# Kernel tuning notes

Measured on AMD Instinct MI355X. Metric: run time of the kernel, lower is better.

## Reference

```python
import jax, jax.numpy as jnp
import numpy as np

V, D, B, T = 50257, 512, 64, 512
MEM, FWD = 64, 48
RETRO = MEM - FWD  # 16
EPS = 1e-5


def setup_inputs() -> dict:
    key = jax.random.key(0)
    ks = jax.random.split(key, 16)
    n = lambda i, shape: (jax.random.normal(ks[i], shape, jnp.float32) * 0.02)
    return dict(
        seq=jax.random.randint(ks[0], (B, T), 0, V),
        embed=n(1, (V, D)),
        ff_w1=n(2, (D, 2 * D)), ff_b1=jnp.zeros((2 * D,), jnp.float32),
        ff_w2=n(3, (2 * D, D)), ff_b2=jnp.zeros((D,), jnp.float32),
        ln_g=jnp.ones((D,), jnp.float32), ln_b=jnp.zeros((D,), jnp.float32),
        fg_w=n(4, (D,)), fg_b=jnp.zeros((), jnp.float32),
        nw_w1=n(5, (2 * D, D)), nw_b1=jnp.zeros((D,), jnp.float32),
        nw_w2=n(6, (D,)), nw_b2=jnp.zeros((), jnp.float32),
        wq=n(7, (D, D)), bq=jnp.zeros((D,), jnp.float32),
        wk=n(8, (D, D)), bk=jnp.zeros((D,), jnp.float32),
        wv=n(9, (D, D)), bv=jnp.zeros((D,), jnp.float32),
        wo=n(10, (D, D)), bo=jnp.zeros((D,), jnp.float32),
        rq_w=n(11, (D, D)), rq_b=jnp.zeros((D,), jnp.float32),
        out_w=n(12, (D, V)), out_b=jnp.zeros((V,), jnp.float32),
    )


def reference(seq, embed, ff_w1, ff_b1, ff_w2, ff_b2, ln_g, ln_b,
              fg_w, fg_b, nw_w1, nw_b1, nw_w2, nw_b2,
              wq, bq, wk, bk, wv, bv, wo, bo, rq_w, rq_b, out_w, out_b):
    Bz = seq.shape[0]
    # Encoder: embed -> FFN residual -> LayerNorm
    h0 = embed[seq]                                            # [B,T,D]
    ff = jax.nn.relu(h0 @ ff_w1 + ff_b1) @ ff_w2 + ff_b2
    x = h0 + ff
    mu = x.mean(-1, keepdims=True)
    var = ((x - mu) ** 2).mean(-1, keepdims=True)
    hidden = (x - mu) / jnp.sqrt(var + EPS) * ln_g + ln_b       # [B,T,D]

    cand = hidden[:, :-3, :]                                   # [B,n_cand,D]
    n_cand = cand.shape[1]
    # Forward-gate topk (sorted ascending, as in torch code)
    fwd_scores = cand @ fg_w + fg_b                            # [B,n_cand]
    _, fwd_idx = jax.lax.top_k(fwd_scores, FWD)
    fwd_idx = jnp.sort(fwd_idx, axis=1)                        # [B,FWD]
    fwd_h = jnp.take_along_axis(hidden, fwd_idx[:, :, None], axis=1)  # [B,FWD,D]

    # Condition 'D': MHA re-encode (1 head) of forward slots over full sequence
    q = fwd_h @ wq + bq                                        # [B,FWD,D]
    kk = hidden @ wk + bk                                      # [B,T,D]
    v = hidden @ wv + bv                                       # [B,T,D]
    attn = jax.nn.softmax(jnp.einsum('bkd,btd->bkt', q, kk) / jnp.sqrt(jnp.float32(D)), axis=-1)
    re_slots = jnp.einsum('bkt,btd->bkd', attn, v) @ wo + bo   # [B,FWD,D]

    # New-write gate over skipped candidates -> retro slots
    context = hidden.mean(1)                                   # [B,D]
    gi = jnp.concatenate([cand, jnp.broadcast_to(context[:, None, :], cand.shape)], axis=-1)
    gs = jax.nn.sigmoid(jax.nn.relu(gi @ nw_w1 + nw_b1) @ nw_w2 + nw_b2)  # [B,n_cand]
    fwd_mask = jnp.zeros((Bz, n_cand), jnp.float32).at[
        jnp.arange(Bz)[:, None], fwd_idx].set(1.0)
    masked = jnp.where(fwd_mask > 0, -1e9, gs)
    _, sel = jax.lax.top_k(masked, RETRO)                      # [B,RETRO], descending-score order
    retro_h = jnp.take_along_axis(hidden, sel[:, :, None], axis=1)  # [B,RETRO,D]

    memory = jnp.concatenate([re_slots, retro_h], axis=1)      # [B,MEM,D] (exactly full)
    mem_mask = jnp.ones((Bz, MEM), jnp.float32)

    # Read head
    qh = hidden[:, -2, :] @ rq_w + rq_b                        # [B,D]
    scores = jnp.einsum('bmd,bd->bm', memory, qh)
    scores = jnp.where(mem_mask == 0, -1e9, scores)
    a = jax.nn.softmax(scores, axis=-1)
    ctx = jnp.einsum('bm,bmd->bd', a, memory)
    return ctx @ out_w + out_b                                 # [B,V]
```

## Files before the change

### kernel.cpp

```cpp
#include <hip/hip_runtime.h>

typedef unsigned short u16;
typedef unsigned int u32;

#define VV 50257
#define NCAND 509
#define NFWD 48
#define NRETRO 16

typedef __attribute__((ext_vector_type(8))) short bf16x8;
typedef __attribute__((ext_vector_type(4))) float f32x4;

__device__ __forceinline__ float bf2f(u16 u) {
  union { u32 i; float f; } v; v.i = ((u32)u) << 16; return v.f;
}
__device__ __forceinline__ u16 f2bf(float f) {
  union { float f; u32 u; } v; v.f = f;
  u32 u = v.u; u += 0x7fffu + ((u >> 16) & 1u); return (u16)(u >> 16);
}
__device__ __forceinline__ u16 bft(float f) {
  union { float f; u32 u; } v; v.f = f; return (u16)(v.u >> 16);
}
__device__ __forceinline__ float ldsel(const void* p, size_t i, int isbf) {
  return isbf ? bf2f(((const u16*)p)[i]) : ((const float*)p)[i];
}

__device__ __forceinline__ void g2l16(const u16* g, u16* l) {
  __builtin_amdgcn_global_load_lds((const __attribute__((address_space(1))) u32*)g,
                                   (__attribute__((address_space(3))) u32*)l, 16, 0, 0);
}

__global__ void detect_k(const u32* __restrict__ w, int* __restrict__ flag) {
  int bf = 1;
  for (int i = 0; i < 16; ++i) {
    u32 b1 = (w[i] >> 8) & 0x7fu;
    if (!(b1 >= 0x30u && b1 < 0x40u)) bf = 0;
  }
  *flag = bf;
}

__global__ void sentinel_k(float* __restrict__ out, int n, float val) {
  int i = blockIdx.x * 256 + threadIdx.x;
  if (i < n) out[i] = val;
}

__global__ __launch_bounds__(256) void tsplit_k(const float* __restrict__ W,
                                                u16* __restrict__ Th, u16* __restrict__ Tl,
                                                int K, int N) {
  __shared__ float tt[32][33];
  int nt = N >> 5;
  int n0 = (blockIdx.x % nt) << 5;
  int k0 = (blockIdx.x / nt) << 5;
  int c = threadIdx.x & 31, r = threadIdx.x >> 5;
#pragma unroll
  for (int i = 0; i < 32; i += 8) tt[r + i][c] = W[(size_t)(k0 + r + i) * N + n0 + c];
  __syncthreads();
#pragma unroll
  for (int i = 0; i < 32; i += 8) {
    int n = n0 + r + i, k = k0 + c;
    float v = tt[c][r + i];
    u16 h = bft(v);
    int idx = n * K + (k & ~63) + ((k & 63) ^ ((n & 7) << 3));
    Th[idx] = h; Tl[idx] = f2bf(v - bf2f(h));
  }
}

__global__ __launch_bounds__(256) void gsplit_k(const float* __restrict__ embed,
                                                const int* __restrict__ seqp,
                                                u16* __restrict__ Ph, u16* __restrict__ Pl) {
  int g = blockIdx.x * 256 + threadIdx.x;
  int m = g >> 6, j8 = (g & 63) << 3;
  const float* s = embed + (size_t)seqp[m] * 512 + j8;
  float4 a = *(const float4*)s;
  float4 b = *(const float4*)(s + 4);
  u16 h0 = bft(a.x), h1 = bft(a.y), h2 = bft(a.z), h3 = bft(a.w);
  u16 h4 = bft(b.x), h5 = bft(b.y), h6 = bft(b.z), h7 = bft(b.w);
  uint4 hv, lv;
  hv.x = (u32)h0 | ((u32)h1 << 16); hv.y = (u32)h2 | ((u32)h3 << 16);
  hv.z = (u32)h4 | ((u32)h5 << 16); hv.w = (u32)h6 | ((u32)h7 << 16);
  lv.x = (u32)f2bf(a.x - bf2f(h0)) | ((u32)f2bf(a.y - bf2f(h1)) << 16);
  lv.y = (u32)f2bf(a.z - bf2f(h2)) | ((u32)f2bf(a.w - bf2f(h3)) << 16);
  lv.z = (u32)f2bf(b.x - bf2f(h4)) | ((u32)f2bf(b.y - bf2f(h5)) << 16);
  lv.w = (u32)f2bf(b.z - bf2f(h6)) | ((u32)f2bf(b.w - bf2f(h7)) << 16);
  int di = m * 512 + (j8 ^ ((m & 7) << 3));
  *(uint4*)&Ph[di] = hv;
  *(uint4*)&Pl[di] = lv;
}

template<int ADDM, int RELU, int ACC, int OUT>
__global__ __launch_bounds__(256) void mgemm_k(
    const u16* __restrict__ Ah, const u16* __restrict__ Al,
    const u16* __restrict__ Bh, const u16* __restrict__ Bl,
    int ldk, int koff,
    const float* __restrict__ biasf, int boff,
    const u16* __restrict__ Rh, const u16* __restrict__ Rl,
    const float* __restrict__ addf,
    float* __restrict__ Cf, u16* __restrict__ Cb,
    u16* __restrict__ Ohi, u16* __restrict__ Olo)
{
  __shared__ __align__(16) u16 lds[32768];
  int tid = threadIdx.x;
  int cpx = gridDim.x >> 3;
  int bid = blockIdx.x;
  int wg = (bid & 7) * cpx + (bid >> 3);
  int my = wg >> 2, nx = wg & 3;
  int m0 = my << 7, n0 = nx << 7;
  int lane = tid & 63, wid = tid >> 6;

  const u16* gw; int stw;
  if (wid == 0)      { gw = Ah + (size_t)m0 * 512;        stw = 512; }
  else if (wid == 1) { gw = Al + (size_t)m0 * 512;        stw = 512; }
  else if (wid == 2) { gw = Bh + (size_t)n0 * ldk + koff; stw = ldk; }
  else               { gw = Bl + (size_t)n0 * ldk + koff; stw = ldk; }
  const u16* gl = gw + (size_t)(lane >> 3) * stw + ((lane & 7) << 3);
  int lb = wid << 13;

  f32x4 acc[4][4] = {};
  int wr = wid >> 1, wc = wid & 1;
  int cl = lane & 15;
  int kq8 = (lane >> 4) << 3;
  int swz = (cl & 7) << 3;

  for (int k0 = 0; k0 < 512; k0 += 64) {
#pragma unroll
    for (int i = 0; i < 16; ++i)
      g2l16(gl + (size_t)(i << 3) * stw + k0, &lds[lb + (i << 9)]);
    __syncthreads();
#pragma unroll
    for (int kt = 0; kt < 2; ++kt) {
      int kA = ((kt << 5) + kq8) ^ swz;
      bf16x8 bh[4], blo[4];
#pragma unroll
      for (int i = 0; i < 4; ++i) {
        int ib = (((wc << 6) + (i << 4) + cl) << 6) + kA;
        bh[i]  = *(const bf16x8*)&lds[16384 + ib];
        blo[i] = *(const bf16x8*)&lds[24576 + ib];
      }
#pragma unroll
      for (int i2 = 0; i2 < 4; ++i2) {
        int ia = (((wr << 6) + (i2 << 4) + cl) << 6) + kA;
        bf16x8 ah  = *(const bf16x8*)&lds[ia];
        bf16x8 alo = *(const bf16x8*)&lds[8192 + ia];
#pragma unroll
        for (int j = 0; j < 4; ++j) {
          acc[i2][j] = __builtin_amdgcn_mfma_f32_16x16x32_bf16(ah,  bh[j],  acc[i2][j], 0, 0, 0);
          acc[i2][j] = __builtin_amdgcn_mfma_f32_16x16x32_bf16(alo, bh[j],  acc[i2][j], 0, 0, 0);
          acc[i2][j] = __builtin_amdgcn_mfma_f32_16x16x32_bf16(ah,  blo[j], acc[i2][j], 0, 0, 0);
        }
      }
    }
    __syncthreads();
  }

  int rq = (lane >> 4) << 2;
  int mb = m0 + (wr << 6);
  int nb = n0 + (wc << 6);
#pragma unroll
  for (int j = 0; j < 4; ++j) {
    int n = nb + (j << 4) + cl;
    float bi = biasf ? biasf[boff + n] : 0.f;
#pragma unroll
    for (int i2 = 0; i2 < 4; ++i2) {
#pragma unroll
      for (int r = 0; r < 4; ++r) {
        int m = mb + (i2 << 4) + rq + r;
        float v = acc[i2][j][r] + bi;
        if (ADDM == 1) {
          int ridx = m * 512 + (n ^ ((m & 7) << 3));
          v += bf2f(Rh[ridx]) + bf2f(Rl[ridx]);
        }
        if (ADDM == 2) v += addf[((m >> 9) << 9) + n];
        if (ACC) v += Cf[(size_t)m * 512 + n];
        if (RELU) v = fmaxf(v, 0.f);
        if (OUT == 0) Cf[(size_t)m * 512 + n] = v;
        else if (OUT == 1) Cb[(size_t)m * 512 + n] = f2bf(v);
        else if (OUT == 2) {
          u16 h = bft(v);
          int oidx = m * 512 + (n ^ ((m & 7) << 3));
          Ohi[oidx] = h; Olo[oidx] = f2bf(v - bf2f(h));
        } else {
          int r64 = (m * 43691) >> 21;
          int mm = (r64 << 6) + (m - r64 * 48);
          Cf[(size_t)mm * 512 + n] = v;
        }
      }
    }
  }
}

template<int AG, int ADDM, int RELU, int ACC, int OUTBF>
__global__ __launch_bounds__(256) void gemm_k(
    const float* __restrict__ A, int lda,
    const void* __restrict__ gbase, const int* __restrict__ gidx,
    const void* __restrict__ Bw, int ldb, size_t boff,
    const void* __restrict__ bias, size_t bias_eoff,
    const void* __restrict__ adg_base, const int* __restrict__ adg_idx, int adg_ld,
    const float* __restrict__ addf, int add_shift, int addf_ld,
    void* __restrict__ Cv, int ldc, int K,
    const int* __restrict__ flagp)
{
  __shared__ float As[16][68];
  __shared__ float Bs[16][68];
  int isbf = *flagp;
  int tid = threadIdx.x;
  int m0 = blockIdx.y * 64;
  int n0 = blockIdx.x * 64;
  int tx = tid & 15, ty = tid >> 4;
  int arow = tid >> 2;
  int akq  = (tid & 3) << 2;
  int bcol = tid & 63;
  int bk0  = tid >> 6;

  size_t a_off;
  if (AG) a_off = (size_t)gidx[m0 + arow] * (size_t)lda;
  else    a_off = (size_t)(m0 + arow) * (size_t)lda;

  float acc[4][4] = {};

  for (int k0 = 0; k0 < K; k0 += 16) {
    {
      float4 v = *(const float4*)(A + a_off + k0 + akq);
      As[akq + 0][arow] = v.x;
      As[akq + 1][arow] = v.y;
      As[akq + 2][arow] = v.z;
      As[akq + 3][arow] = v.w;
    }
    if (isbf) {
      const u16* bp = (const u16*)Bw + boff;
#pragma unroll
      for (int l = 0; l < 4; ++l) {
        int kb = bk0 + (l << 2);
        Bs[kb][bcol] = bf2f(bp[(size_t)(k0 + kb) * ldb + n0 + bcol]);
      }
    } else {
      const float* bp = (const float*)Bw + boff;
#pragma unroll
      for (int l = 0; l < 4; ++l) {
        int kb = bk0 + (l << 2);
        Bs[kb][bcol] = bp[(size_t)(k0 + kb) * ldb + n0 + bcol];
      }
    }
    __syncthreads();
#pragma unroll
    for (int k = 0; k < 16; ++k) {
      float4 a4 = *(const float4*)&As[k][ty << 2];
      float4 b4 = *(const float4*)&Bs[k][tx << 2];
      float a[4] = {a4.x, a4.y, a4.z, a4.w};
      float bv[4] = {b4.x, b4.y, b4.z, b4.w};
#pragma unroll
      for (int i = 0; i < 4; ++i)
#pragma unroll
        for (int j = 0; j < 4; ++j) acc[i][j] += a[i] * bv[j];
    }
    __syncthreads();
  }

  int mrow = m0 + (ty << 2);
  int ncol = n0 + (tx << 2);
  float bi4[4] = {0.f, 0.f, 0.f, 0.f};
  if (bias) {
#pragma unroll
    for (int j = 0; j < 4; ++j) bi4[j] = ldsel(bias, bias_eoff + ncol + j, isbf);
  }
#pragma unroll
  for (int i = 0; i < 4; ++i) {
    int m = mrow + i;
    float v[4];
#pragma unroll
    for (int j = 0; j < 4; ++j) v[j] = acc[i][j] + bi4[j];
// ... 59 lines not shown
    const u16* ph = Hh + (size_t)grow * 512;
    const u16* pl = Hl + (size_t)grow * 512;
    float s = 0.f;
#pragma unroll
    for (int d = 0; d < 8; ++d) {
      float hv = bf2f(ph[lx + d * 64]) + bf2f(pl[lx + d * 64]);
      ca[d] += hv;
      s += hv * wl[lane + d * 64];
    }
#pragma unroll
    for (int off = 32; off > 0; off >>= 1) s += __shfl_xor(s, off);
    if (lane == 0) out[bb * 512 + t0 + r] = s + bias;
  }
#pragma unroll
  for (int d = 0; d < 8; ++d) cred[wave][lane + d * 64] = ca[d];
  __syncthreads();
  for (int d = threadIdx.x; d < 512; d += 256)
    part[(size_t)((bb << 3) + blockIdx.x) * 512 + d] =
        cred[0][d] + cred[1][d] + cred[2][d] + cred[3][d];
}

template<int SIG>
__global__ __launch_bounds__(256) void score_k(const float* __restrict__ h,
                                               const void* __restrict__ w,
                                               const void* __restrict__ b,
                                               float* __restrict__ out,
                                               const int* __restrict__ flagp) {
  int isbf = *flagp;
  int bb = blockIdx.y; int t0 = blockIdx.x * 64;
  __shared__ float wl[512];
  for (int d = threadIdx.x; d < 512; d += 256) wl[d] = ldsel(w, d, isbf);
  __syncthreads();
  int wave = threadIdx.x >> 6, lane = threadIdx.x & 63;
  float bias = ldsel(b, 0, isbf);
  for (int r = wave; r < 64; r += 4) {
    const float* hp = h + ((size_t)bb * 512 + t0 + r) * 512;
    float s = 0.f;
#pragma unroll
    for (int d = 0; d < 8; ++d) s += hp[lane + d * 64] * wl[lane + d * 64];
#pragma unroll
    for (int off = 32; off > 0; off >>= 1) s += __shfl_xor(s, off);
    if (lane == 0) {
      float v = s + bias;
      if (SIG) v = 1.0f / (1.0f + expf(-v));
      out[bb * 512 + t0 + r] = v;
    }
  }
}

__global__ __launch_bounds__(256) void topk_fwd_k(const float* __restrict__ scores,
                                                  int* __restrict__ fwd_idx,
                                                  int* __restrict__ fwd_mask) {
  int b = blockIdx.x, tid = threadIdx.x;
  __shared__ float vals[512];
  __shared__ float rv[256];
  __shared__ int   ri[256];
  __shared__ int   selb[NFWD];
  for (int t = tid; t < 512; t += 256) {
    vals[t] = (t < NCAND) ? scores[b * 512 + t] : -3.0e38f;
    fwd_mask[b * 512 + t] = 0;
  }
  __syncthreads();
  for (int it = 0; it < NFWD; ++it) {
    float bv = -3.0e38f; int bi = 0x7fffffff;
    for (int t = tid; t < 512; t += 256) {
      float v = vals[t];
      if (v > bv || (v == bv && t < bi)) { bv = v; bi = t; }
    }
    rv[tid] = bv; ri[tid] = bi;
    __syncthreads();
    for (int s = 128; s > 0; s >>= 1) {
      if (tid < s) {
        float ov = rv[tid + s]; int oi = ri[tid + s];
        if (ov > rv[tid] || (ov == rv[tid] && oi < ri[tid])) { rv[tid] = ov; ri[tid] = oi; }
      }
      __syncthreads();
    }
    if (tid == 0) { selb[it] = ri[0]; vals[ri[0]] = -3.0e38f; }
    __syncthreads();
  }
  if (tid == 0) {
    for (int i = 1; i < NFWD; ++i) {
      int v = selb[i], j = i - 1;
      while (j >= 0 && selb[j] > v) { selb[j + 1] = selb[j]; --j; }
      selb[j + 1] = v;
    }
    for (int i = 0; i < NFWD; ++i) {
      fwd_idx[b * NFWD + i] = selb[i];
      fwd_mask[b * 512 + selb[i]] = 1;
    }
  }
}

__global__ __launch_bounds__(256) void topk_retro_k(const float* __restrict__ gs,
                                                    const int* __restrict__ fwd_mask,
                                                    int* __restrict__ sel) {
  int b = blockIdx.x, tid = threadIdx.x;
  __shared__ float vals[512];
  __shared__ float rv[256];
  __shared__ int   ri[256];
  for (int t = tid; t < 512; t += 256) {
    float v;
    if (t < NCAND) v = fwd_mask[b * 512 + t] ? -1.0e9f : gs[b * 512 + t];
    else v = -3.0e38f;
    vals[t] = v;
  }
  __syncthreads();
  for (int it = 0; it < NRETRO; ++it) {
    float bv = -3.0e38f; int bi = 0x7fffffff;
    for (int t = tid; t < 512; t += 256) {
      float v = vals[t];
      if (v > bv || (v == bv && t < bi)) { bv = v; bi = t; }
    }
    rv[tid] = bv; ri[tid] = bi;
    __syncthreads();
    for (int s = 128; s > 0; s >>= 1) {
      if (tid < s) {
        float ov = rv[tid + s]; int oi = ri[tid + s];
        if (ov > rv[tid] || (ov == rv[tid] && oi < ri[tid])) { rv[tid] = ov; ri[tid] = oi; }
      }
      __syncthreads();
    }
    if (tid == 0) { sel[b * NRETRO + it] = ri[0]; vals[ri[0]] = -3.0e38f; }
    __syncthreads();
  }
}

__global__ __launch_bounds__(512) void context_red_k(const float* __restrict__ part,
                                                     float* __restrict__ ctx) {
  int b = blockIdx.x, d = threadIdx.x;
  float s = 0.f;
#pragma unroll
  for (int c = 0; c < 8; ++c) s += part[(size_t)((b << 3) + c) * 512 + d];
  ctx[b * 512 + d] = s * (1.0f / 512.0f);
}

__global__ __launch_bounds__(256) void fwdh_gather_p(const u16* __restrict__ Hh,
                                                     const u16* __restrict__ Hl,
                                                     const int* __restrict__ fwd_idx,
                                                     u16* __restrict__ Fh, u16* __restrict__ Fl) {
  int idx = blockIdx.x * 256 + threadIdx.x;
  int d = idx & 511, r = idx >> 9;
  int b = r / NFWD, i = r % NFWD;
  int t = fwd_idx[b * NFWD + i];
  int srow = b * 512 + t;
  int si = srow * 512 + (d & ~63) + ((d & 63) ^ ((srow & 7) << 3));
  float v = bf2f(Hh[si]) + bf2f(Hl[si]);
  u16 h = bft(v);
  int di = r * 512 + (d & ~63) + ((d & 63) ^ ((r & 7) << 3));
  Fh[di] = h; Fl[di] = f2bf(v - bf2f(h));
}

__global__ __launch_bounds__(256) void retro_gather_p(const u16* __restrict__ Hh,
                                                      const u16* __restrict__ Hl,
                                                      const int* __restrict__ sel,
                                                      float* __restrict__ mem) {
  int idx = blockIdx.x * 256 + threadIdx.x;
  int d = idx & 511, r = idx >> 9, b = r >> 4, j = r & 15;
  int t = sel[b * NRETRO + j];
  int srow = b * 512 + t;
  int si = srow * 512 + (d & ~63) + ((d & 63) ^ ((srow & 7) << 3));
  mem[((size_t)b * 64 + NFWD + j) * 512 + d] = bf2f(Hh[si]) + bf2f(Hl[si]);
}

__global__ __launch_bounds__(256) void s_k(const float* __restrict__ q,
                                           const u16* __restrict__ kk,
                                           float* __restrict__ S) {
  int b = blockIdx.y, t0 = blockIdx.x * 64;
  int tid = threadIdx.x, tq = tid & 15, kq = tid >> 4;
  __shared__ float qs[16][49];
  __shared__ float ks[16][68];
  float acc[3][4] = {};
  for (int dc = 0; dc < 512; dc += 16) {
    for (int e = tid; e < 768; e += 256) {
      int d = e / 48, k2 = e % 48;
      qs[d][k2] = q[((size_t)b * 48 + k2) * 512 + dc + d];
    }
    for (int e = tid; e < 1024; e += 256) {
      int t = e >> 4, d = e & 15;
      ks[d][t] = bf2f(kk[((size_t)b * 512 + t0 + t) * 512 + dc + d]);
    }
    __syncthreads();
#pragma unroll
    for (int d = 0; d < 16; ++d) {
      float4 kv = *(const float4*)&ks[d][tq << 2];
#pragma unroll
      for (int j = 0; j < 3; ++j) {
        float qv = qs[d][kq * 3 + j];
        acc[j][0] += qv * kv.x; acc[j][1] += qv * kv.y;
        acc[j][2] += qv * kv.z; acc[j][3] += qv * kv.w;
      }
    }
    __syncthreads();
  }
  const float sc = 0.044194173824159216f;
#pragma unroll
  for (int j = 0; j < 3; ++j) {
    int k = kq * 3 + j;
    float4 o; o.x = acc[j][0] * sc; o.y = acc[j][1] * sc;
    o.z = acc[j][2] * sc; o.w = acc[j][3] * sc;
    *(float4*)&S[((size_t)b * 48 + k) * 512 + t0 + (tq << 2)] = o;
  }
}

__global__ __launch_bounds__(256) void softmax_k(float* __restrict__ S) {
  float* p = S + (size_t)blockIdx.x * 512;
  int tid = threadIdx.x;
  __shared__ float red[256];
  __shared__ float stat[2];
  float v0 = p[tid], v1 = p[tid + 256];
  red[tid] = fmaxf(v0, v1);
  __syncthreads();
  for (int s = 128; s > 0; s >>= 1) { if (tid < s) red[tid] = fmaxf(red[tid], red[tid + s]); __syncthreads(); }
  if (tid == 0) stat[0] = red[0];
  __syncthreads();
  float mx = stat[0];
  float e0 = expf(v0 - mx), e1 = expf(v1 - mx);
  red[tid] = e0 + e1;
  __syncthreads();
  for (int s = 128; s > 0; s >>= 1) { if (tid < s) red[tid] += red[tid + s]; __syncthreads(); }
  if (tid == 0) stat[1] = 1.0f / red[0];
  __syncthreads();
  float inv = stat[1];
  p[tid] = e0 * inv; p[tid + 256] = e1 * inv;
}

__global__ __launch_bounds__(256) void pv_k(const float* __restrict__ P,
                                            const u16* __restrict__ vvp,
                                            u16* __restrict__ Ph, u16* __restrict__ Pl) {
  int b = blockIdx.y, d0 = blockIdx.x * 64;
  int tid = threadIdx.x, dq = tid & 15, kq = tid >> 4;
  __shared__ float ps[16][49];
  __shared__ float vs[16][68];
  float acc[3][4] = {};
  for (int tc = 0; tc < 512; tc += 16) {
    for (int e = tid; e < 768; e += 256) {
      int t = e / 48, k2 = e % 48;
      ps[t][k2] = P[((size_t)b * 48 + k2) * 512 + tc + t];
    }
    for (int e = tid; e < 1024; e += 256) {
      int t = e >> 6, d = e & 63;
      vs[t][d] = bf2f(vvp[((size_t)b * 512 + tc + t) * 512 + d0 + d]);
    }
    __syncthreads();
#pragma unroll
    for (int t = 0; t < 16; ++t) {
      float4 vval = *(const float4*)&vs[t][dq << 2];
#pragma unroll
      for (int j = 0; j < 3; ++j) {
        float pp = ps[t][kq * 3 + j];
        acc[j][0] += pp * vval.x; acc[j][1] += pp * vval.y;
        acc[j][2] += pp * vval.z; acc[j][3] += pp * vval.w;
      }
    }
    __syncthreads();
  }
#pragma unroll
  for (int j = 0; j < 3; ++j) {
    int k = kq * 3 + j;
    int row = b * 48 + k;
    int c = (row & 7) << 3;
    int di = row * 512 + d0 + ((dq << 2) ^ c);
    float v0 = acc[j][0], v1 = acc[j][1], v2 = acc[j][2], v3 = acc[j][3];
    u16 h0 = bft(v0), h1 = bft(v1), h2 = bft(v2), h3 = bft(v3);
    uint2 hv, lv;
    hv.x = (u32)h0 | ((u32)h1 << 16); hv.y = (u32)h2 | ((u32)h3 << 16);
    lv.x = (u32)f2bf(v0 - bf2f(h0)) | ((u32)f2bf(v1 - bf2f(h1)) << 16);
    lv.y = (u32)f2bf(v2 - bf2f(h2)) | ((u32)f2bf(v3 - bf2f(h3)) << 16);
    *(uint2*)&Ph[di] = hv;
    *(uint2*)&Pl[di] = lv;
  }
}

__global__ __launch_bounds__(512) void qh_p_k(const u16* __restrict__ Hh,
                                              const u16* __restrict__ Hl,
                                              const float* __restrict__ rq_w,
                                              const float* __restrict__ rq_b,
                                              float* __restrict__ qh) {
  int b = blockIdx.x, d = threadIdx.x;
  __shared__ float hr[512];
  int row = b * 512 + 510;
  int idx = row * 512 + (d & ~63) + ((d & 63) ^ 48);
  hr[d] = bf2f(Hh[idx]) + bf2f(Hl[idx]);
  __syncthreads();
  float s = 0.f;
  for (int k = 0; k < 512; ++k) s += hr[k] * rq_w[(size_t)k * 512 + d];
  qh[b * 512 + d] = s + rq_b[d];
}

__global__ __launch_bounds__(512) void mem_attn_k(const float* __restrict__ mem,
                                                  const float* __restrict__ qh,
                                                  float* __restrict__ ctx,
                                                  float* __restrict__ ctxT) {
  int b = blockIdx.x, tid = threadIdx.x;
  __shared__ float qv[512];
  __shared__ float sc[64];
  qv[tid] = qh[b * 512 + tid];
  __syncthreads();
  if (tid < 64) {
    const float* mp = mem + ((size_t)b * 64 + tid) * 512;
    float s = 0.f;
    for (int d = 0; d < 512; ++d) s += mp[d] * qv[d];
    float mx = s;
#pragma unroll
    for (int off = 32; off > 0; off >>= 1) mx = fmaxf(mx, __shfl_xor(mx, off));
    float e = expf(s - mx);
    float sum = e;
#pragma unroll
    for (int off = 32; off > 0; off >>= 1) sum += __shfl_xor(sum, off);
    sc[tid] = e / sum;
  }
  __syncthreads();
  float a = 0.f;
  for (int m = 0; m < 64; ++m) a += sc[m] * mem[((size_t)b * 64 + m) * 512 + tid];
  ctx[b * 512 + tid] = a;
  ctxT[(size_t)tid * 64 + b] = a;
}

__global__ __launch_bounds__(256) void out_part_k(const float* __restrict__ ctxT,
                                                  const float* __restrict__ out_w,
                                                  float* __restrict__ P0,
                                                  float* __restrict__ P1) {
  int bid = blockIdx.x;
  int slab2 = (bid & 7) + ((bid >> 6) << 3);
  if (slab2 >= 394) return;
  int xslab = slab2 >> 1, kh = slab2 & 1;
  int bg = (bid >> 3) & 7;
  int n = xslab * 256 + threadIdx.x;
  int nc = n < VV ? n : VV - 1;
  int b0 = bg << 3;
  int k0 = kh << 8;
  float acc[8] = {};
  const float* wp = out_w + (size_t)k0 * VV;
#pragma unroll 8
  for (int k = 0; k < 256; ++k) {
    float w = wp[(size_t)k * VV + nc];
    const float* cp = ctxT + ((size_t)(k0 + k) << 6) + b0;
#pragma unroll
    for (int i = 0; i < 8; ++i) acc[i] += cp[i] * w;
  }
  float* dst = kh ? P1 : P0;
  if (n < VV) {
#pragma unroll
    for (int i = 0; i < 8; ++i) dst[(size_t)(b0 + i) * VV + n] = acc[i];
  }
}

__global__ __launch_bounds__(256) void out_comb_k(const float* __restrict__ P0,
                                                  const float* __restrict__ P1,
                                                  const float* __restrict__ ob,
                                                  float* __restrict__ out) {
  int b = blockIdx.y;
  int n = blockIdx.x * 256 + threadIdx.x;
  if (n < VV) {
    size_t i = (size_t)b * VV + n;
    out[i] = P0[i] + P1[i] + ob[n];
  }
}

extern "C" void kernel_launch(void* const* d_in, const int* in_sizes, int n_in,
                              void* d_out, int out_size, void* d_ws, size_t ws_size,
                              hipStream_t stream) {
  const int*  seq    = (const int*)d_in[0];
  const void* embed  = d_in[1];
  const void* ff_w1  = d_in[2];
  const void* ff_b1  = d_in[3];
  const void* ff_w2  = d_in[4];
  const void* ff_b2  = d_in[5];
  const void* ln_g   = d_in[6];
  const void* ln_b   = d_in[7];
  const void* fg_w   = d_in[8];
  const void* fg_b   = d_in[9];
  const void* nw_w1  = d_in[10];
  const void* nw_b1  = d_in[11];
  const void* nw_w2  = d_in[12];
  const void* nw_b2  = d_in[13];
  const void* wq     = d_in[14];
  const void* bq     = d_in[15];
  const void* wk     = d_in[16];
  const void* bk     = d_in[17];
  const void* wv     = d_in[18];
  const void* bv     = d_in[19];
  const void* wo     = d_in[20];
  const void* bo     = d_in[21];
  const void* rq_w   = d_in[22];
  const void* rq_b   = d_in[23];
  const void* out_w  = d_in[24];
  const void* out_b  = d_in[25];
  float* out = (float*)d_out;

  float* ws = (float*)d_ws;
  float* hidden = ws;
  float* g1f    = ws;
  u16*   kku    = (u16*)ws;
  u16*   vvu    = (u16*)(ws + 8388608);
  float* P0     = ws;
  float* P1     = ws + 3216448;
  u16* actHh = (u16*)(ws + 16777216);
  u16* actHl = actHh + 8388608;
  u16* h0h   = (u16*)(ws + 25165824);
  u16* h0l   = h0h + 8388608;
  u16* Hh    = (u16*)(ws + 16777216);
  u16* Hl    = Hh + 16777216;
  size_t S0 = 33554432;
  float* fwd_scores = ws + S0;
  float* gs         = ws + S0 + 32768;
  float* context    = ws + S0 + 65536;
  float* gate_bias  = ws + S0 + 98304;
  float* qh         = ws + S0 + 131072;
  float* ctx        = ws + S0 + 163840;
  int*   fwd_idx    = (int*)(ws + S0 + 196608);
  int*   sel        = (int*)(ws + S0 + 199680);
  int*   fwd_mask   = (int*)(ws + S0 + 200704);
  int*   flagp      = (int*)(ws + S0 + 233472);
  float* cpart      = ws + S0 + 262144;
  u16*   Fh         = (u16*)(ws + S0 + 262144);
  u16*   Fl         = Fh + 1572864;
  float* q          = ws + S0 + 1835008;
  float* Smat       = ws + S0 + 3407872;
  u16* W0   = (u16*)(ws + S0 + 3407872);
  u16* WTnh = W0;            u16* WTnl = W0 + 262144;
  u16* WTkh = W0 + 524288;   u16* WTkl = W0 + 786432;
  u16* WTvh = W0 + 1048576;  u16* WTvl = W0 + 1310720;
  u16* WT1h = W0 + 1572864;  u16* WT1l = W0 + 2097152;
  u16* WT2h = W0 + 2621440;  u16* WT2l = W0 + 3145728;
  u16* Ph   = (u16*)(ws + S0 + 4980736);
  u16* Pl   = Ph + 1572864;
  u16* Wq0  = (u16*)(ws + S0 + 6553600);
  u16* WTqh = Wq0;          u16* WTql = Wq0 + 262144;
  u16* WToh = Wq0 + 524288; u16* WTol = Wq0 + 786432;
  float* memory = ws + S0 + 8126464;
  float* ctxT   = fwd_scores;
  const size_t NEED = (size_t)(33554432 + 10223616) * 4;

  if (ws_size < NEED) {
    float val = 500.0f + (float)(ws_size >> 20);
    sentinel_k<<<(out_size + 255) / 256, 256, 0, stream>>>(out, out_size, val);
    return;
  }

  detect_k<<<1, 1, 0, stream>>>((const u32*)embed, flagp);

  tsplit_k<<<512, 256, 0, stream>>>((const float*)ff_w1, WT1h, WT1l, 512, 1024);
  tsplit_k<<<512, 256, 0, stream>>>((const float*)ff_w2, WT2h, WT2l, 1024, 512);
  tsplit_k<<<256, 256, 0, stream>>>((const float*)nw_w1, WTnh, WTnl, 512, 512);
  tsplit_k<<<256, 256, 0, stream>>>((const float*)wk,    WTkh, WTkl, 512, 512);
  tsplit_k<<<256, 256, 0, stream>>>((const float*)wv,    WTvh, WTvl, 512, 512);
  tsplit_k<<<256, 256, 0, stream>>>((const float*)wq,    WTqh, WTql, 512, 512);
  tsplit_k<<<256, 256, 0, stream>>>((const float*)wo,    WToh, WTol, 512, 512);

  for (int mc = 0; mc < 2; ++mc) {
    const int* seqp = seq + mc * 16384;
    float* hid = hidden + (size_t)mc * 16384 * 512;
    gsplit_k<<<4096, 256, 0, stream>>>((const float*)embed, seqp, h0h, h0l);
    mgemm_k<0,1,0,2><<<512, 256, 0, stream>>>(h0h, h0l, WT1h, WT1l, 512, 0,
        (const float*)ff_b1, 0, nullptr, nullptr, nullptr,
        nullptr, nullptr, actHh, actHl);
    mgemm_k<0,0,0,0><<<512, 256, 0, stream>>>(actHh, actHl, WT2h, WT2l, 1024, 0,
        nullptr, 0, nullptr, nullptr, nullptr,
        hid, nullptr, nullptr, nullptr);
    mgemm_k<0,1,0,2><<<512, 256, 0, stream>>>(h0h, h0l, WT1h + 512*512, WT1l + 512*512, 512, 0,
        (const float*)ff_b1, 512, nullptr, nullptr, nullptr,
        nullptr, nullptr, actHh, actHl);
    mgemm_k<1,0,1,0><<<512, 256, 0, stream>>>(actHh, actHl, WT2h, WT2l, 1024, 512,
        (const float*)ff_b2, 0, h0h, h0l, nullptr,
        hid, nullptr, nullptr, nullptr);
  }
  ln_split_k<<<32768, 256, 0, stream>>>(hidden, (const float*)ln_g, (const float*)ln_b, Hh, Hl);
  gatectx_k<<<dim3(8,64), 256, 0, stream>>>(Hh, Hl, (const float*)fg_w, (const float*)fg_b,
                                            fwd_scores, cpart);
  topk_fwd_k<<<64, 256, 0, stream>>>(fwd_scores, fwd_idx, fwd_mask);
  context_red_k<<<64, 512, 0, stream>>>(cpart, context);
  gemm_k<0,0,0,0,0><<<dim3(8,1), 256, 0, stream>>>(
      context, 512, nullptr, nullptr, nw_w1, 512, (size_t)512*512, nw_b1, 0,
      nullptr, nullptr, 0, nullptr, 0, 0, gate_bias, 512, 512, flagp);
  mgemm_k<2,1,0,0><<<1024, 256, 0, stream>>>(Hh, Hl, WTnh, WTnl, 512, 0,
      nullptr, 0, nullptr, nullptr, gate_bias,
      g1f, nullptr, nullptr, nullptr);
  score_k<1><<<dim3(8,64), 256, 0, stream>>>(g1f, nw_w2, nw_b2, gs, flagp);
  topk_retro_k<<<64, 256, 0, stream>>>(gs, fwd_mask, sel);
  retro_gather_p<<<2048, 256, 0, stream>>>(Hh, Hl, sel, memory);
  fwdh_gather_p<<<6144, 256, 0, stream>>>(Hh, Hl, fwd_idx, Fh, Fl);
  mgemm_k<0,0,0,0><<<96, 256, 0, stream>>>(Fh, Fl, WTqh, WTql, 512, 0,
      (const float*)bq, 0, nullptr, nullptr, nullptr,
      q, nullptr, nullptr, nullptr);
  mgemm_k<0,0,0,1><<<1024, 256, 0, stream>>>(Hh, Hl, WTkh, WTkl, 512, 0,
      (const float*)bk, 0, nullptr, nullptr, nullptr,
      nullptr, kku, nullptr, nullptr);
  mgemm_k<0,0,0,1><<<1024, 256, 0, stream>>>(Hh, Hl, WTvh, WTvl, 512, 0,
      (const float*)bv, 0, nullptr, nullptr, nullptr,
      nullptr, vvu, nullptr, nullptr);
  s_k<<<dim3(8,64), 256, 0, stream>>>(q, kku, Smat);
  softmax_k<<<3072, 256, 0, stream>>>(Smat);
  pv_k<<<dim3(8,64), 256, 0, stream>>>(Smat, vvu, Ph, Pl);
  mgemm_k<0,0,0,3><<<96, 256, 0, stream>>>(Ph, Pl, WToh, WTol, 512, 0,
      (const float*)bo, 0, nullptr, nullptr, nullptr,
      memory, nullptr, nullptr, nullptr);
  qh_p_k<<<64, 512, 0, stream>>>(Hh, Hl, (const float*)rq_w, (const float*)rq_b, qh);
  mem_attn_k<<<64, 512, 0, stream>>>(memory, qh, ctx, ctxT);
  out_part_k<<<3200, 256, 0, stream>>>(ctxT, (const float*)out_w, P0, P1);
  out_comb_k<<<dim3(197,64), 256, 0, stream>>>(P0, P1, (const float*)out_b, out);
}
```

Baseline: 1.254 ms.

## Fuse FFN and K/V GEMMs, rank-based top-k, MFMA output projection

Generalizes the split-bf16 MFMA GEMM with N-tile count, K-steps and output stride. This lets the FFN run as one wide W1 GEMM and one full-K W2 GEMM over four M chunks, and lets K and V be computed by one concatenated GEMM. The iterative argmax top-k loops become a single-pass rank-counting selection. The fp32 output projection (partial sums plus combine) is replaced by a bf16-transposed out_w and an MFMA GEMM that uses a hi/lo split of ctx. The out_w transpose now runs on every call and out_w carries only a single bf16 term, which reduces precision on that operand.

```diff
diff --git a/kernel.cpp b/kernel.cpp
--- a/kernel.cpp
+++ b/kernel.cpp
@@ -63,6 +63,32 @@
     int idx = n * K + (k & ~63) + ((k & 63) ^ ((n & 7) << 3));
     Th[idx] = h; Tl[idx] = f2bf(v - bf2f(h));
   }
+}
+
+__global__ __launch_bounds__(256) void tout_k(const float* __restrict__ W,
+                                              u16* __restrict__ WoT) {
+  __shared__ float tt[32][33];
+  const int nt = 1572;
+  int n0 = (blockIdx.x % nt) << 5;
+  int k0 = (blockIdx.x / nt) << 5;
+  int c = threadIdx.x & 31, r = threadIdx.x >> 5;
+#pragma unroll
+  for (int i = 0; i < 32; i += 8) {
+    int n = n0 + c;
+    tt[r + i][c] = (n < VV) ? W[(size_t)(k0 + r + i) * VV + n] : 0.f;
+  }
+  __syncthreads();
+#pragma unroll
+  for (int i = 0; i < 32; i += 8) {
+    int n = n0 + r + i, k = k0 + c;
+    WoT[(size_t)n * 512 + (k & ~63) + ((k & 63) ^ ((n & 7) << 3))] = f2bf(tt[c][r + i]);
+  }
+}
+
+__global__ void concat2_k(const float* __restrict__ a, const float* __restrict__ b,
+                          float* __restrict__ o) {
+  int i = blockIdx.x * 256 + threadIdx.x;
+  if (i < 1024) o[i] = (i < 512) ? a[i] : b[i - 512];
 }
 
 __global__ __launch_bounds__(256) void gsplit_k(const float* __restrict__ embed,
@@ -87,31 +113,31 @@
   *(uint4*)&Pl[di] = lv;
 }
 
-template<int ADDM, int RELU, int ACC, int OUT>
+template<int NT, int KST, int ADDM, int RELU, int OUT>
 __global__ __launch_bounds__(256) void mgemm_k(
     const u16* __restrict__ Ah, const u16* __restrict__ Al,
     const u16* __restrict__ Bh, const u16* __restrict__ Bl,
-    int ldk, int koff,
+    int lda, int ldb, int koff,
     const float* __restrict__ biasf, int boff,
     const u16* __restrict__ Rh, const u16* __restrict__ Rl,
     const float* __restrict__ addf,
     float* __restrict__ Cf, u16* __restrict__ Cb,
-    u16* __restrict__ Ohi, u16* __restrict__ Olo)
+    u16* __restrict__ Ohi, u16* __restrict__ Olo, int ldc)
 {
   __shared__ __align__(16) u16 lds[32768];
   int tid = threadIdx.x;
   int cpx = gridDim.x >> 3;
   int bid = blockIdx.x;
   int wg = (bid & 7) * cpx + (bid >> 3);
-  int my = wg >> 2, nx = wg & 3;
+  int my = wg / NT, nx = wg % NT;
   int m0 = my << 7, n0 = nx << 7;
   int lane = tid & 63, wid = tid >> 6;
 
   const u16* gw; int stw;
-  if (wid == 0)      { gw = Ah + (size_t)m0 * 512;        stw = 512; }
-  else if (wid == 1) { gw = Al + (size_t)m0 * 512;        stw = 512; }
-  else if (wid == 2) { gw = Bh + (size_t)n0 * ldk + koff; stw = ldk; }
-  else               { gw = Bl + (size_t)n0 * ldk + koff; stw = ldk; }
+  if (wid == 0)      { gw = Ah + (size_t)m0 * lda;        stw = lda; }
+  else if (wid == 1) { gw = Al + (size_t)m0 * lda;        stw = lda; }
+  else if (wid == 2) { gw = Bh + (size_t)n0 * ldb + koff; stw = ldb; }
+  else               { gw = Bl + (size_t)n0 * ldb + koff; stw = ldb; }
   const u16* gl = gw + (size_t)(lane >> 3) * stw + ((lane & 7) << 3);
   int lb = wid << 13;
 
@@ -121,7 +147,7 @@
   int kq8 = (lane >> 4) << 3;
   int swz = (cl & 7) << 3;
 
-  for (int k0 = 0; k0 < 512; k0 += 64) {
+  for (int k0 = 0; k0 < KST * 64; k0 += 64) {
 #pragma unroll
     for (int i = 0; i < 16; ++i)
       g2l16(gl + (size_t)(i << 3) * stw + k0, &lds[lb + (i << 9)]);
@@ -170,13 +196,12 @@
           v += bf2f(Rh[ridx]) + bf2f(Rl[ridx]);
         }
         if (ADDM == 2) v += addf[((m >> 9) << 9) + n];
-        if (ACC) v += Cf[(size_t)m * 512 + n];
         if (RELU) v = fmaxf(v, 0.f);
-        if (OUT == 0) Cf[(size_t)m * 512 + n] = v;
-        else if (OUT == 1) Cb[(size_t)m * 512 + n] = f2bf(v);
+        if (OUT == 0) Cf[(size_t)m * ldc + n] = v;
+        else if (OUT == 1) Cb[(size_t)m * ldc + n] = f2bf(v);
         else if (OUT == 2) {
           u16 h = bft(v);
-          int oidx = m * 512 + (n ^ ((m & 7) << 3));
+          size_t oidx = (size_t)m * ldc + (n & ~63) + ((n & 63) ^ ((m & 7) << 3));
           Ohi[oidx] = h; Olo[oidx] = f2bf(v - bf2f(h));
         } else {
           int r64 = (m * 43691) >> 21;
@@ -184,6 +209,70 @@
           Cf[(size_t)mm * 512 + n] = v;
         }
       }
+    }
+  }
+}
+
+__global__ __launch_bounds__(256) void out_mgemm_k(
+    const u16* __restrict__ ctxh, const u16* __restrict__ ctxl,
+    const u16* __restrict__ WoT, const float* __restrict__ ob,
+    float* __restrict__ out) {
+  __shared__ __align__(16) u16 lds[16384];
+  int tid = threadIdx.x;
+  int n0 = blockIdx.x << 7;
+  int lane = tid & 63, wid = tid >> 6;
+  const u16* gw; int lb0;
+  if (wid == 0)      { gw = ctxh;                         lb0 = 0; }
+  else if (wid == 1) { gw = ctxl;                         lb0 = 4096; }
+  else if (wid == 2) { gw = WoT + (size_t)n0 * 512;        lb0 = 8192; }
+  else               { gw = WoT + (size_t)(n0 + 64) * 512; lb0 = 12288; }
+  const u16* gl = gw + (size_t)(lane >> 3) * 512 + ((lane & 7) << 3);
+
+  f32x4 acc[4][2] = {};
+  int cl = lane & 15;
+  int kq8 = (lane >> 4) << 3;
+  int swz = (cl & 7) << 3;
+
+  for (int k0 = 0; k0 < 512; k0 += 64) {
+#pragma unroll
+    for (int i = 0; i < 8; ++i)
+      g2l16(gl + (size_t)(i << 3) * 512 + k0, &lds[lb0 + (i << 9)]);
+    __syncthreads();
+#pragma unroll
+    for (int kt = 0; kt < 2; ++kt) {
+      int kA = ((kt << 5) + kq8) ^ swz;
+      bf16x8 bw[2];
+#pragma unroll
+      for (int j = 0; j < 2; ++j) {
+        int rB = (wid << 5) + (j << 4) + cl;
+        bw[j] = *(const bf16x8*)&lds[8192 + (rB << 6) + kA];
+      }
+#pragma unroll
+      for (int i2 = 0; i2 < 4; ++i2) {
+        int ra = ((i2 << 4) + cl) << 6;
+        bf16x8 ah  = *(const bf16x8*)&lds[ra + kA];
+        bf16x8 alo = *(const bf16x8*)&lds[4096 + ra + kA];
+#pragma unroll
+        for (int j = 0; j < 2; ++j) {
+          acc[i2][j] = __builtin_amdgcn_mfma_f32_16x16x32_bf16(ah,  bw[j], acc[i2][j], 0, 0, 0);
+          acc[i2][j] = __builtin_amdgcn_mfma_f32_16x16x32_bf16(alo, bw[j], acc[i2][j], 0, 0, 0);
+        }
+      }
+    }
+    __syncthreads();
+  }
+
+  int rq = (lane >> 4) << 2;
+#pragma unroll
+  for (int j = 0; j < 2; ++j) {
+    int n = n0 + (wid << 5) + (j << 4) + cl;
+    if (n < VV) {
+      float bi = ob[n];
+#pragma unroll
+      for (int i2 = 0; i2 < 4; ++i2)
+#pragma unroll
+        for (int r = 0; r < 4; ++r)
+          out[(size_t)((i2 << 4) + rq + r) * VV + n] = acc[i2][j][r] + bi;
     }
   }
 }
@@ -211,10 +300,7 @@
   int bcol = tid & 63;
   int bk0  = tid >> 6;
 
-  size_t a_off;
-  if (AG) a_off = (size_t)gidx[m0 + arow] * (size_t)lda;
-  else    a_off = (size_t)(m0 + arow) * (size_t)lda;
-
+  size_t a_off = (size_t)(m0 + arow) * (size_t)lda;
   float acc[4][4] = {};
 
   for (int k0 = 0; k0 < K; k0 += 16) {
@@ -380,42 +466,37 @@
                                                   int* __restrict__ fwd_idx,
                                                   int* __restrict__ fwd_mask) {
   int b = blockIdx.x, tid = threadIdx.x;
-  __shared__ float vals[512];
-  __shared__ float rv[256];
-  __shared__ int   ri[256];
-  __shared__ int   selb[NFWD];
-  for (int t = tid; t < 512; t += 256) {
-    vals[t] = (t < NCAND) ? scores[b * 512 + t] : -3.0e38f;
-    fwd_mask[b * 512 + t] = 0;
-  }
-  __syncthreads();
-  for (int it = 0; it < NFWD; ++it) {
-    float bv = -3.0e38f; int bi = 0x7fffffff;
-    for (int t = tid; t < 512; t += 256) {
-      float v = vals[t];
-      if (v > bv || (v == bv && t < bi)) { bv = v; bi = t; }
-    }
-    rv[tid] = bv; ri[tid] = bi;
-    __syncthreads();
-    for (int s = 128; s > 0; s >>= 1) {
-      if (tid < s) {
-        float ov = rv[tid + s]; int oi = ri[tid + s];
-        if (ov > rv[tid] || (ov == rv[tid] && oi < ri[tid])) { rv[tid] = ov; ri[tid] = oi; }
-      }
-      __syncthreads();
-    }
-    if (tid == 0) { selb[it] = ri[0]; vals[ri[0]] = -3.0e38f; }
-    __syncthreads();
-  }
-  if (tid == 0) {
-    for (int i = 1; i < NFWD; ++i) {
-      int v = selb[i], j = i - 1;
-      while (j >= 0 && selb[j] > v) { selb[j + 1] = selb[j]; --j; }
-      selb[j + 1] = v;
-    }
-    for (int i = 0; i < NFWD; ++i) {
-      fwd_idx[b * NFWD + i] = selb[i];
-      fwd_mask[b * 512 + selb[i]] = 1;
+  __shared__ float sv[512];
+  __shared__ int flg[512];
+  for (int t = tid; t < 512; t += 256)
+    sv[t] = (t < NCAND) ? scores[b * 512 + t] : -3.0e38f;
+  __syncthreads();
+  const float4* sv4 = (const float4*)sv;
+#pragma unroll
+  for (int h = 0; h < 2; ++h) {
+    int t = tid + (h << 8);
+    float s = sv[t];
+    int cnt = 0;
+    for (int t2 = 0; t2 < 128; ++t2) {
+      float4 o = sv4[t2];
+      int base = t2 << 2;
+      cnt += (o.x > s) || (o.x == s && (base + 0) < t);
+      cnt += (o.y > s) || (o.y == s && (base + 1) < t);
+      cnt += (o.z > s) || (o.z == s && (base + 2) < t);
+      cnt += (o.w > s) || (o.w == s && (base + 3) < t);
+    }
+    int f = (cnt < NFWD) ? 1 : 0;
+    flg[t] = f;
+    fwd_mask[b * 512 + t] = f;
+  }
+  __syncthreads();
+#pragma unroll
+  for (int h = 0; h < 2; ++h) {
+    int t = tid + (h << 8);
+    if (flg[t]) {
+      int pos = 0;
+      for (int t2 = 0; t2 < t; ++t2) pos += flg[t2];
+      fwd_idx[b * NFWD + pos] = t;
     }
   }
 }
@@ -424,33 +505,29 @@
                                                     const int* __restrict__ fwd_mask,
                                                     int* __restrict__ sel) {
   int b = blockIdx.x, tid = threadIdx.x;
-  __shared__ float vals[512];
-  __shared__ float rv[256];
-  __shared__ int   ri[256];
+  __shared__ float sv[512];
   for (int t = tid; t < 512; t += 256) {
     float v;
     if (t < NCAND) v = fwd_mask[b * 512 + t] ? -1.0e9f : gs[b * 512 + t];
     else v = -3.0e38f;
-    vals[t] = v;
-  }
-  __syncthreads();
-  for (int it = 0; it < NRETRO; ++it) {
-    float bv = -3.0e38f; int bi = 0x7fffffff;
-    for (int t = tid; t < 512; t += 256) {
-      float v = vals[t];
-      if (v > bv || (v == bv && t < bi)) { bv = v; bi = t; }
-    }
-    rv[tid] = bv; ri[tid] = bi;
-    __syncthreads();
-    for (int s = 128; s > 0; s >>= 1) {
-      if (tid < s) {
-        float ov = rv[tid + s]; int oi = ri[tid + s];
-        if (ov > rv[tid] || (ov == rv[tid] && oi < ri[tid])) { rv[tid] = ov; ri[tid] = oi; }
-      }
-      __syncthreads();
-    }
-    if (tid == 0) { sel[b * NRETRO + it] = ri[0]; vals[ri[0]] = -3.0e38f; }
-    __syncthreads();
+    sv[t] = v;
+  }
+  __syncthreads();
+  const float4* sv4 = (const float4*)sv;
+#pragma unroll
+  for (int h = 0; h < 2; ++h) {
+    int t = tid + (h << 8);
+    float s = sv[t];
+    int cnt = 0;
+    for (int t2 = 0; t2 < 128; ++t2) {
+      float4 o = sv4[t2];
+      int base = t2 << 2;
+      cnt += (o.x > s) || (o.x == s && (base + 0) < t);
+      cnt += (o.y > s) || (o.y == s && (base + 1) < t);
+      cnt += (o.z > s) || (o.z == s && (base + 2) < t);
+      cnt += (o.w > s) || (o.w == s && (base + 3) < t);
+    }
+    if (cnt < NRETRO) sel[b * NRETRO + cnt] = t;
   }
 }
 
@@ -506,7 +583,7 @@
     }
     for (int e = tid; e < 1024; e += 256) {
       int t = e >> 4, d = e & 15;
-      ks[d][t] = bf2f(kk[((size_t)b * 512 + t0 + t) * 512 + dc + d]);
+      ks[d][t] = bf2f(kk[((size_t)b * 512 + t0 + t) * 1024 + dc + d]);
     }
     __syncthreads();
 #pragma unroll
@@ -568,7 +645,7 @@
     }
     for (int e = tid; e < 1024; e += 256) {
       int t = e >> 6, d = e & 63;
-      vs[t][d] = bf2f(vvp[((size_t)b * 512 + tc + t) * 512 + d0 + d]);
+      vs[t][d] = bf2f(vvp[((size_t)b * 512 + tc + t) * 1024 + d0 + d]);
     }
     __syncthreads();
 #pragma unroll
@@ -618,8 +695,8 @@
 
 __global__ __launch_bounds__(512) void mem_attn_k(const float* __restrict__ mem,
                                                   const float* __restrict__ qh,
-                                                  float* __restrict__ ctx,
-                                                  float* __restrict__ ctxT) {
+                                                  u16* __restrict__ ctxh,
+                                                  u16* __restrict__ ctxl) {
   int b = blockIdx.x, tid = threadIdx.x;
   __shared__ float qv[512];
   __shared__ float sc[64];
@@ -641,49 +718,9 @@
   __syncthreads();
   float a = 0.f;
   for (int m = 0; m < 64; ++m) a += sc[m] * mem[((size_t)b * 64 + m) * 512 + tid];
-  ctx[b * 512 + tid] = a;
-  ctxT[(size_t)tid * 64 + b] = a;
-}
-
-__global__ __launch_bounds__(256) void out_part_k(const float* __restrict__ ctxT,
-                                                  const float* __restrict__ out_w,
-                                                  float* __restrict__ P0,
-                                                  float* __restrict__ P1) {
-  int bid = blockIdx.x;
-  int slab2 = (bid & 7) + ((bid >> 6) << 3);
-  if (slab2 >= 394) return;
-  int xslab = slab2 >> 1, kh = slab2 & 1;
-  int bg = (bid >> 3) & 7;
-  int n = xslab * 256 + threadIdx.x;
-  int nc = n < VV ? n : VV - 1;
-  int b0 = bg << 3;
-  int k0 = kh << 8;
-  float acc[8] = {};
-  const float* wp = out_w + (size_t)k0 * VV;
-#pragma unroll 8
-  for (int k = 0; k < 256; ++k) {
-    float w = wp[(size_t)k * VV + nc];
-    const float* cp = ctxT + ((size_t)(k0 + k) << 6) + b0;
-#pragma unroll
-    for (int i = 0; i < 8; ++i) acc[i] += cp[i] * w;
-  }
-  float* dst = kh ? P1 : P0;
-  if (n < VV) {
-#pragma unroll
-    for (int i = 0; i < 8; ++i) dst[(size_t)(b0 + i) * VV + n] = acc[i];
-  }
-}
-
-__global__ __launch_bounds__(256) void out_comb_k(const float* __restrict__ P0,
-                                                  const float* __restrict__ P1,
-                                                  const float* __restrict__ ob,
-                                                  float* __restrict__ out) {
-  int b = blockIdx.y;
-  int n = blockIdx.x * 256 + threadIdx.x;
-  if (n < VV) {
-    size_t i = (size_t)b * VV + n;
-    out[i] = P0[i] + P1[i] + ob[n];
-  }
+  int di = b * 512 + (tid & ~63) + ((tid & 63) ^ ((b & 7) << 3));
+  u16 h = bft(a);
+  ctxh[di] = h; ctxl[di] = f2bf(a - bf2f(h));
 }
 
 extern "C" void kernel_launch(void* const* d_in, const int* in_sizes, int n_in,
@@ -720,45 +757,43 @@
   float* ws = (float*)d_ws;
   float* hidden = ws;
   float* g1f    = ws;
-  u16*   kku    = (u16*)ws;
-  u16*   vvu    = (u16*)(ws + 8388608);
-  float* P0     = ws;
-  float* P1     = ws + 3216448;
-  u16* actHh = (u16*)(ws + 16777216);
+  u16*   kvu    = (u16*)ws;
+  u16* h0h   = (u16*)(ws + 16777216);
+  u16* h0l   = h0h + 4194304;
+  u16* actHh = (u16*)(ws + 20971520);
   u16* actHl = actHh + 8388608;
-  u16* h0h   = (u16*)(ws + 25165824);
-  u16* h0l   = h0h + 8388608;
   u16* Hh    = (u16*)(ws + 16777216);
   u16* Hl    = Hh + 16777216;
+  u16* WoT   = (u16*)(ws + 16777216);
   size_t S0 = 33554432;
   float* fwd_scores = ws + S0;
   float* gs         = ws + S0 + 32768;
   float* context    = ws + S0 + 65536;
   float* gate_bias  = ws + S0 + 98304;
   float* qh         = ws + S0 + 131072;
-  float* ctx        = ws + S0 + 163840;
+  u16*   ctxh       = (u16*)(ws + S0 + 163840);
+  u16*   ctxl       = ctxh + 32768;
   int*   fwd_idx    = (int*)(ws + S0 + 196608);
   int*   sel        = (int*)(ws + S0 + 199680);
   int*   fwd_mask   = (int*)(ws + S0 + 200704);
   int*   flagp      = (int*)(ws + S0 + 233472);
+  float* bkv        = ws + S0 + 236544;
   float* cpart      = ws + S0 + 262144;
   u16*   Fh         = (u16*)(ws + S0 + 262144);
   u16*   Fl         = Fh + 1572864;
   float* q          = ws + S0 + 1835008;
   float* Smat       = ws + S0 + 3407872;
-  u16* W0   = (u16*)(ws + S0 + 3407872);
-  u16* WTnh = W0;            u16* WTnl = W0 + 262144;
-  u16* WTkh = W0 + 524288;   u16* WTkl = W0 + 786432;
-  u16* WTvh = W0 + 1048576;  u16* WTvl = W0 + 1310720;
-  u16* WT1h = W0 + 1572864;  u16* WT1l = W0 + 2097152;
-  u16* WT2h = W0 + 2621440;  u16* WT2l = W0 + 3145728;
-  u16* Ph   = (u16*)(ws + S0 + 4980736);
-  u16* Pl   = Ph + 1572864;
-  u16* Wq0  = (u16*)(ws + S0 + 6553600);
-  u16* WTqh = Wq0;          u16* WTql = Wq0 + 262144;
-  u16* WToh = Wq0 + 524288; u16* WTol = Wq0 + 786432;
+  u16* W0    = (u16*)(ws + S0 + 3407872);
+  u16* WTnh  = W0;            u16* WTnl  = W0 + 262144;
+  u16* WTkvh = W0 + 524288;   u16* WTkvl = W0 + 1048576;
+  u16* WT1h  = W0 + 1572864;  u16* WT1l  = W0 + 2097152;
+  u16* WT2h  = W0 + 2621440;  u16* WT2l  = W0 + 3145728;
+  u16* Ph    = (u16*)(ws + S0 + 4980736);
+  u16* Pl    = Ph + 1572864;
+  u16* Wq0   = (u16*)(ws + S0 + 6553600);
+  u16* WTqh  = Wq0;          u16* WTql = Wq0 + 262144;
+  u16* WToh  = Wq0 + 524288; u16* WTol = Wq0 + 786432;
   float* memory = ws + S0 + 8126464;
-  float* ctxT   = fwd_scores;
   const size_t NEED = (size_t)(33554432 + 10223616) * 4;
 
   if (ws_size < NEED) {
@@ -772,27 +807,24 @@
   tsplit_k<<<512, 256, 0, stream>>>((const float*)ff_w1, WT1h, WT1l, 512, 1024);
   tsplit_k<<<512, 256, 0, stream>>>((const float*)ff_w2, WT2h, WT2l, 1024, 512);
   tsplit_k<<<256, 256, 0, stream>>>((const float*)nw_w1, WTnh, WTnl, 512, 512);
-  tsplit_k<<<256, 256, 0, stream>>>((const float*)wk,    WTkh, WTkl, 512, 512);
-  tsplit_k<<<256, 256, 0, stream>>>((const float*)wv,    WTvh, WTvl, 512, 512);
-  tsplit_k<<<256, 256, 0, stream>>>((const float*)wq,    WTqh, WTql, 512, 512);
-  tsplit_k<<<256, 256, 0, stream>>>((const float*)wo,    WToh, WTol, 512, 512);
-
-  for (int mc = 0; mc < 2; ++mc) {
-    const int* seqp = seq + mc * 16384;
-    float* hid = hidden + (size_t)mc * 16384 * 512;
-    gsplit_k<<<4096, 256, 0, stream>>>((const float*)embed, seqp, h0h, h0l);
-    mgemm_k<0,1,0,2><<<512, 256, 0, stream>>>(h0h, h0l, WT1h, WT1l, 512, 0,
+  tsplit_k<<<256, 256, 0, stream>>>((const float*)wk, WTkvh, WTkvl, 512, 512);
+  tsplit_k<<<256, 256, 0, stream>>>((const float*)wv, WTkvh + 512*512, WTkvl + 512*512, 512, 512);
+  tsplit_k<<<256, 256, 0, stream>>>((const float*)wq, WTqh, WTql, 512, 512);
+  tsplit_k<<<256, 256, 0, stream>>>((const float*)wo, WToh, WTol, 512, 512);
+  concat2_k<<<4, 256, 0, stream>>>((const float*)bk, (const float*)bv, bkv);
+
+  for (int mc = 0; mc < 4; ++mc) {
+    const int* seqp = seq + mc * 8192;
+    float* hid = hidden + (size_t)mc * 8192 * 512;
+    gsplit_k<<<2048, 256, 0, stream>>>((const float*)embed, seqp, h0h, h0l);
+    mgemm_k<8,8,0,1,2><<<512, 256, 0, stream>>>(
+        h0h, h0l, WT1h, WT1l, 512, 512, 0,
         (const float*)ff_b1, 0, nullptr, nullptr, nullptr,
-        nullptr, nullptr, actHh, actHl);
-    mgemm_k<0,0,0,0><<<512, 256, 0, stream>>>(actHh, actHl, WT2h, WT2l, 1024, 0,
-        nullptr, 0, nullptr, nullptr, nullptr,
-        hid, nullptr, nullptr, nullptr);
-    mgemm_k<0,1,0,2><<<512, 256, 0, stream>>>(h0h, h0l, WT1h + 512*512, WT1l + 512*512, 512, 0,
-        (const float*)ff_b1, 512, nullptr, nullptr, nullptr,
-        nullptr, nullptr, actHh, actHl);
-    mgemm_k<1,0,1,0><<<512, 256, 0, stream>>>(actHh, actHl, WT2h, WT2l, 1024, 512,
+        nullptr, nullptr, actHh, actHl, 1024);
+    mgemm_k<4,16,1,0,0><<<256, 256, 0, stream>>>(
+        actHh, actHl, WT2h, WT2l, 1024, 1024, 0,
         (const float*)ff_b2, 0, h0h, h0l, nullptr,
-        hid, nullptr, nullptr, nullptr);
+        hid, nullptr, nullptr, nullptr, 512);
   }
   ln_split_k<<<32768, 256, 0, stream>>>(hidden, (const float*)ln_g, (const float*)ln_b, Hh, Hl);
   gatectx_k<<<dim3(8,64), 256, 0, stream>>>(Hh, Hl, (const float*)fg_w, (const float*)fg_b,
@@ -802,30 +834,31 @@
   gemm_k<0,0,0,0,0><<<dim3(8,1), 256, 0, stream>>>(
       context, 512, nullptr, nullptr, nw_w1, 512, (size_t)512*512, nw_b1, 0,
       nullptr, nullptr, 0, nullptr, 0, 0, gate_bias, 512, 512, flagp);
-  mgemm_k<2,1,0,0><<<1024, 256, 0, stream>>>(Hh, Hl, WTnh, WTnl, 512, 0,
+  mgemm_k<4,8,2,1,0><<<1024, 256, 0, stream>>>(
+      Hh, Hl, WTnh, WTnl, 512, 512, 0,
       nullptr, 0, nullptr, nullptr, gate_bias,
-      g1f, nullptr, nullptr, nullptr);
+      g1f, nullptr, nullptr, nullptr, 512);
   score_k<1><<<dim3(8,64), 256, 0, stream>>>(g1f, nw_w2, nw_b2, gs, flagp);
   topk_retro_k<<<64, 256, 0, stream>>>(gs, fwd_mask, sel);
   retro_gather_p<<<2048, 256, 0, stream>>>(Hh, Hl, sel, memory);
   fwdh_gather_p<<<6144, 256, 0, stream>>>(Hh, Hl, fwd_idx, Fh, Fl);
-  mgemm_k<0,0,0,0><<<96, 256, 0, stream>>>(Fh, Fl, WTqh, WTql, 512, 0,
+  mgemm_k<4,8,0,0,0><<<96, 256, 0, stream>>>(
+      Fh, Fl, WTqh, WTql, 512, 512, 0,
       (const float*)bq, 0, nullptr, nullptr, nullptr,
-      q, nullptr, nullptr, nullptr);
-  mgemm_k<0,0,0,1><<<1024, 256, 0, stream>>>(Hh, Hl, WTkh, WTkl, 512, 0,
-      (const float*)bk, 0, nullptr, nullptr, nullptr,
-      nullptr, kku, nullptr, nullptr);
-  mgemm_k<0,0,0,1><<<1024, 256, 0, stream>>>(Hh, Hl, WTvh, WTvl, 512, 0,
-      (const float*)bv, 0, nullptr, nullptr, nullptr,
-      nullptr, vvu, nullptr, nullptr);
-  s_k<<<dim3(8,64), 256, 0, stream>>>(q, kku, Smat);
+      q, nullptr, nullptr, nullptr, 512);
+  mgemm_k<8,8,0,0,1><<<2048, 256, 0, stream>>>(
+      Hh, Hl, WTkvh, WTkvl, 512, 512, 0,
+      bkv, 0, nullptr, nullptr, nullptr,
+      nullptr, kvu, nullptr, nullptr, 1024);
+  s_k<<<dim3(8,64), 256, 0, stream>>>(q, kvu, Smat);
   softmax_k<<<3072, 256, 0, stream>>>(Smat);
-  pv_k<<<dim3(8,64), 256, 0, stream>>>(Smat, vvu, Ph, Pl);
-  mgemm_k<0,0,0,3><<<96, 256, 0, stream>>>(Ph, Pl, WToh, WTol, 512, 0,
+  pv_k<<<dim3(8,64), 256, 0, stream>>>(Smat, kvu + 512, Ph, Pl);
+  mgemm_k<4,8,0,0,3><<<96, 256, 0, stream>>>(
+      Ph, Pl, WToh, WTol, 512, 512, 0,
       (const float*)bo, 0, nullptr, nullptr, nullptr,
-      memory, nullptr, nullptr, nullptr);
+      memory, nullptr, nullptr, nullptr, 512);
   qh_p_k<<<64, 512, 0, stream>>>(Hh, Hl, (const float*)rq_w, (const float*)rq_b, qh);
-  mem_attn_k<<<64, 512, 0, stream>>>(memory, qh, ctx, ctxT);
-  out_part_k<<<3200, 256, 0, stream>>>(ctxT, (const float*)out_w, P0, P1);
-  out_comb_k<<<dim3(197,64), 256, 0, stream>>>(P0, P1, (const float*)out_b, out);
-}
+  mem_attn_k<<<64, 512, 0, stream>>>(memory, qh, ctxh, ctxl);
+  tout_k<<<16 * 1572, 256, 0, stream>>>((const float*)out_w, WoT);
+  out_mgemm_k<<<393, 256, 0, stream>>>(ctxh, ctxl, WoT, (const float*)out_b, out);
+}
```

Result: faster. 1.193 ms (-4.9%).
